# Kernel tuning notes

Measured on AMD Instinct MI355X. Metric: run time of the kernel, lower is better.

## Reference

```python
import jax, jax.numpy as jnp
import numpy as np
from functools import partial

L, B, D_IN, D_MODEL, D_OUT, D_STATE = 2048, 8, 128, 256, 32, 16
D_INNER, DT_RANK, K_CONV = 2 * D_MODEL, D_MODEL // 16, 4
LOG2PI = float(np.log(2.0 * np.pi))


def setup_inputs() -> dict:
    key = jax.random.key(0)
    ks = jax.random.split(key, 16)
    sc = 0.02
    inp = {
        "s": jax.random.normal(ks[0], (L, B, D_IN), jnp.float32),
        "a": jax.random.normal(ks[1], (L, B, D_OUT), jnp.float32),
        # embedding linear
        "W_emb": jax.random.normal(ks[2], (D_IN, D_MODEL), jnp.float32) * sc,
        "b_emb": jnp.zeros((D_MODEL,), jnp.float32),
        # mamba block params
        "norm_w": jnp.ones((D_MODEL,), jnp.float32),
        "W_in": jax.random.normal(ks[3], (D_MODEL, 2 * D_INNER), jnp.float32) * sc,
        "conv_w": jax.random.normal(ks[4], (D_INNER, 1, K_CONV), jnp.float32) * sc,
        "conv_b": jnp.zeros((D_INNER,), jnp.float32),
        "W_x": jax.random.normal(ks[5], (D_INNER, DT_RANK + 2 * D_STATE), jnp.float32) * sc,
        "W_dt": jax.random.normal(ks[6], (DT_RANK, D_INNER), jnp.float32) * sc,
        "b_dt": jnp.full((D_INNER,), -2.0, jnp.float32),  # softplus(-2) ~ small init dt
        "A_log": jnp.broadcast_to(jnp.log(jnp.arange(1, D_STATE + 1, dtype=jnp.float32)), (D_INNER, D_STATE)).copy(),
        "D": jnp.ones((D_INNER,), jnp.float32),
        "W_out": jax.random.normal(ks[7], (D_INNER, D_MODEL), jnp.float32) * sc,
        # action head + log_std
        "W_head": jax.random.normal(ks[8], (D_MODEL, D_OUT), jnp.float32) * sc,
        "b_head": jnp.zeros((D_OUT,), jnp.float32),
        "log_std": jnp.zeros((D_OUT,), jnp.float32),
    }
    return inp


def _rmsnorm(x, w, eps=1e-5):
    return x * jax.lax.rsqrt(jnp.mean(x * x, axis=-1, keepdims=True) + eps) * w


def _silu(x):
    return x * jax.nn.sigmoid(x)


def _mamba_block(x, norm_w, W_in, conv_w, conv_b, W_x, W_dt, b_dt, A_log, D, W_out):
    # x: (B, L, d_model)
    resid = x
    xn = _rmsnorm(x, norm_w)
    xz = xn @ W_in                                  # (B, L, 2*d_inner)
    xp, z = jnp.split(xz, 2, axis=-1)
    # causal depthwise conv over time
    xc = jax.lax.conv_general_dilated(
        xp.transpose(0, 2, 1), conv_w, window_strides=(1,),
        padding=[(K_CONV - 1, 0)], feature_group_count=D_INNER,
        dimension_numbers=("NCH", "OIH", "NCH"))
    xp = _silu((xc + conv_b[None, :, None]).transpose(0, 2, 1))  # (B, L, d_inner)
    # input-dependent SSM params
    x_dbl = xp @ W_x                                # (B, L, dt_rank + 2*d_state)
    dt, Bm, Cm = jnp.split(x_dbl, [DT_RANK, DT_RANK + D_STATE], axis=-1)
    dt = jax.nn.softplus(dt @ W_dt + b_dt)          # (B, L, d_inner)
    A = -jnp.exp(A_log)                             # (d_inner, d_state)

    def step(h, t):
        dt_t, B_t, C_t, x_t = t                     # (B,d_i) (B,d_s) (B,d_s) (B,d_i)
        dA = jnp.exp(dt_t[..., None] * A)           # (B, d_inner, d_state)
        dBx = (dt_t * x_t)[..., None] * B_t[:, None, :]
        h = dA * h + dBx
        y = jnp.einsum("bds,bs->bd", h, C_t)
        return h, y

    h0 = jnp.zeros((x.shape[0], D_INNER, D_STATE), x.dtype)
    tm = lambda u: jnp.moveaxis(u, 1, 0)            # time-major
    _, ys = jax.lax.scan(step, h0, (tm(dt), tm(Bm), tm(Cm), tm(xp)))
    y = jnp.moveaxis(ys, 0, 1) + xp * D             # (B, L, d_inner)
    y = y * _silu(z)
    return y @ W_out + resid


def reference(s, a, W_emb, b_emb, norm_w, W_in, conv_w, conv_b, W_x, W_dt, b_dt,
              A_log, D, W_out, W_head, b_head, log_std):
    x = s @ W_emb + b_emb                           # (L, B, d_model)
    x = x.transpose(1, 0, 2)                        # (B, L, d_model)
    x = _mamba_block(x, norm_w, W_in, conv_w, conv_b, W_x, W_dt, b_dt, A_log, D, W_out)
    x = x.transpose(1, 0, 2)                        # (L, B, d_model)
    mu = x @ W_head + b_head                        # (L, B, d_out)
    # Normal(mu, exp(log_std)).log_prob(a).sum(-1)
    z = (a - mu) * jnp.exp(-log_std)
    logp = -0.5 * z * z - log_std - 0.5 * LOG2PI
    return logp.sum(axis=-1)                        # (L, B)
```

## Files before the change

### kernel.cpp

```cpp
#include <hip/hip_runtime.h>

typedef unsigned short u16;
typedef short bf16x8 __attribute__((ext_vector_type(8)));
typedef float floatx4 __attribute__((ext_vector_type(4)));

#define LSEQ 2048
#define BB 8
#define NTOK (LSEQ*BB)
#define DMODEL 256
#define DINNER 512
#define NSEG 128
#define SEGLEN 16

__device__ __forceinline__ float siluf(float x){ return x / (1.f + __expf(-x)); }
__device__ __forceinline__ float b2f(u16 x){ return __uint_as_float(((unsigned)x) << 16); }
__device__ __forceinline__ u16 f2b(float f){
  unsigned u = __float_as_uint(f);
  unsigned r = (u + 0x7fffu + ((u >> 16) & 1u)) >> 16;
  return (u16)r;
}

__device__ __forceinline__ void compute_dA(float dt, float As0, bool uni,
    const float* __restrict__ Alog, int c, float* dA)
{
  if (uni) {
    float p = __expf(dt*As0);
    float p2 = p*p, p4 = p2*p2, p8 = p4*p4;
    dA[0]=p;      dA[1]=p2;     dA[2]=p2*p;   dA[3]=p4;
    dA[4]=p4*p;   dA[5]=p4*p2;  dA[6]=p4*p2*p;dA[7]=p8;
    dA[8]=p8*p;   dA[9]=p8*p2;  dA[10]=p8*p2*p; dA[11]=p8*p4;
    dA[12]=p8*p4*p; dA[13]=p8*p4*p2; dA[14]=p8*p4*p2*p; dA[15]=p8*p8;
  } else {
    #pragma unroll
    for (int s = 0; s < 16; ++s) dA[s] = __expf(dt * (-__expf(Alog[c*16+s])));
  }
}

__global__ __launch_bounds__(256) void prep_k(
    const float* __restrict__ Wemb, const float* __restrict__ Win,
    const float* __restrict__ Wout, const float* __restrict__ Wx,
    const float* __restrict__ Wh,
    u16* __restrict__ WTe, u16* __restrict__ WTi, u16* __restrict__ WTo,
    u16* __restrict__ WxT, u16* __restrict__ WhT)
{
  int g = blockIdx.x, tid = threadIdx.x;
  if (g < 128) {
    int idx = g*256 + tid; int n = idx >> 7, k = idx & 127;
    WTe[idx] = f2b(Wemb[(size_t)k*256 + n]);
  } else if (g < 1152) {
    int idx = (g-128)*256 + tid; int n = idx >> 8, k = idx & 255;
    WTi[idx] = f2b(Win[(size_t)k*1024 + n]);
  } else if (g < 1664) {
    int idx = (g-1152)*256 + tid; int n = idx >> 9, k = idx & 511;
    WTo[idx] = f2b(Wout[(size_t)k*256 + n]);
  } else if (g < 1760) {
    int idx = (g-1664)*256 + tid; int n = idx >> 9, k = idx & 511;
    WxT[idx] = f2b(Wx[(size_t)k*48 + n]);
  } else {
    int idx = (g-1760)*256 + tid; int j = idx >> 8, k = idx & 255;
    WhT[idx] = f2b(Wh[(size_t)k*32 + j]);
  }
}

__global__ __launch_bounds__(256) void embnorm_k(
    const float* __restrict__ s, const u16* __restrict__ WTe,
    const float* __restrict__ bemb, const float* __restrict__ nw,
    u16* __restrict__ Xb, u16* __restrict__ XNb)
{
  __shared__ u16 SH[64*264];
  __shared__ float ssq[64*4];
  __shared__ float rr[64];
  u16* As = SH;
  u16* Bs = SH + 64*40;
  const int tid = threadIdx.x;
  const int wave = tid >> 6, lane = tid & 63;
  const int quad = lane >> 4, l16 = lane & 15;
  const int m0 = blockIdx.x*64;
  const int wn = wave*64;
  const int srow = tid >> 2, sch = (tid & 3)*8;
  floatx4 acc[4][4];
  #pragma unroll
  for (int r = 0; r < 4; ++r)
    #pragma unroll
    for (int c = 0; c < 4; ++c) acc[r][c] = (floatx4){0.f,0.f,0.f,0.f};

  for (int k0 = 0; k0 < 128; k0 += 32) {
    {
      float4 v0 = *(const float4*)&s[(size_t)(m0+srow)*128 + k0 + sch];
      float4 v1 = *(const float4*)&s[(size_t)(m0+srow)*128 + k0 + sch + 4];
      __align__(16) u16 o[8];
      o[0]=f2b(v0.x); o[1]=f2b(v0.y); o[2]=f2b(v0.z); o[3]=f2b(v0.w);
      o[4]=f2b(v1.x); o[5]=f2b(v1.y); o[6]=f2b(v1.z); o[7]=f2b(v1.w);
      *(uint4*)&As[srow*40 + sch] = *(const uint4*)o;
    }
    #pragma unroll
    for (int p = 0; p < 4; ++p) {
      int row = srow + p*64;
      *(uint4*)&Bs[row*40 + sch] = *(const uint4*)&WTe[(size_t)row*128 + k0 + sch];
    }
    __syncthreads();
    bf16x8 af[4], bf[4];
    #pragma unroll
    for (int r = 0; r < 4; ++r) af[r] = *(const bf16x8*)&As[(r*16 + l16)*40 + quad*8];
    #pragma unroll
    for (int c = 0; c < 4; ++c) bf[c] = *(const bf16x8*)&Bs[(wn + c*16 + l16)*40 + quad*8];
    #pragma unroll
    for (int r = 0; r < 4; ++r)
      #pragma unroll
      for (int c = 0; c < 4; ++c)
        acc[r][c] = __builtin_amdgcn_mfma_f32_16x16x32_bf16(af[r], bf[c], acc[r][c], 0, 0, 0);
    __syncthreads();
  }
  u16* Xs = SH;
  #pragma unroll
  for (int c = 0; c < 4; ++c) {
    int n = wn + c*16 + l16;
    float bv = bemb[n];
    #pragma unroll
    for (int r = 0; r < 4; ++r)
      #pragma unroll
      for (int reg = 0; reg < 4; ++reg) {
        int ml = r*16 + quad*4 + reg;
        Xs[ml*264 + n] = f2b(acc[r][c][reg] + bv);
      }
  }
  __syncthreads();
  #pragma unroll
  for (int p = 0; p < 8; ++p) {
    int row = p*8 + (tid >> 5);
    int col = (tid & 31)*8;
    *(uint4*)&Xb[(size_t)(m0+row)*256 + col] = *(const uint4*)&Xs[row*264 + col];
  }
  const int tk = tid >> 2, q = tid & 3;
  float ss = 0.f;
  #pragma unroll
  for (int j = 0; j < 8; ++j) {
    uint4 v = *(const uint4*)&Xs[tk*264 + q*64 + j*8];
    const u16* u = (const u16*)&v;
    #pragma unroll
    for (int i = 0; i < 8; ++i) { float x = b2f(u[i]); ss += x*x; }
  }
  ssq[tk*4 + q] = ss;
  __syncthreads();
  if (q == 0)
    rr[tk] = rsqrtf((ssq[tk*4]+ssq[tk*4+1]+ssq[tk*4+2]+ssq[tk*4+3])*(1.f/DMODEL) + 1e-5f);
  __syncthreads();
  float r = rr[tk];
  #pragma unroll
  for (int j = 0; j < 8; ++j) {
    int idx = q*64 + j*8;
    uint4 v = *(const uint4*)&Xs[tk*264 + idx];
    const u16* u = (const u16*)&v;
    float4 w0 = *(const float4*)&nw[idx];
    float4 w1 = *(const float4*)&nw[idx+4];
    __align__(16) u16 o[8];
    o[0]=f2b(b2f(u[0])*r*w0.x); o[1]=f2b(b2f(u[1])*r*w0.y);
    o[2]=f2b(b2f(u[2])*r*w0.z); o[3]=f2b(b2f(u[3])*r*w0.w);
    o[4]=f2b(b2f(u[4])*r*w1.x); o[5]=f2b(b2f(u[5])*r*w1.y);
    o[6]=f2b(b2f(u[6])*r*w1.z); o[7]=f2b(b2f(u[7])*r*w1.w);
    *(uint4*)&XNb[(size_t)(m0+tk)*256 + idx] = *(const uint4*)o;
  }
}

template<int K>
__global__ __launch_bounds__(256) void gemm_mfma(
    const u16* __restrict__ Ab, const u16* __restrict__ WT,
    u16* __restrict__ Cv, int N)
{
  __shared__ u16 SH[2*128*72];
  u16* As = SH;
  u16* Bs = SH + 128*72;
  const int tid = threadIdx.x;
  const int wave = tid >> 6, lane = tid & 63;
  const int quad = lane >> 4, l16 = lane & 15;
  const int bm0 = blockIdx.x*128, bn0 = blockIdx.y*128;
  const int wm = (wave & 1)*64, wn = (wave >> 1)*64;
  const int srow = tid >> 3, sch = (tid & 7)*8;
  floatx4 acc[4][4];
  #pragma unroll
  for (int r = 0; r < 4; ++r)
    #pragma unroll
    for (int c = 0; c < 4; ++c) acc[r][c] = (floatx4){0.f,0.f,0.f,0.f};

  for (int k0 = 0; k0 < K; k0 += 64) {
    #pragma unroll
    for (int p = 0; p < 4; ++p) {
      int row = srow + p*32;
      *(uint4*)&As[row*72 + sch] = *(const uint4*)&Ab[(size_t)(bm0+row)*K + k0 + sch];
      *(uint4*)&Bs[row*72 + sch] = *(const uint4*)&WT[(size_t)(bn0+row)*K + k0 + sch];
    }
    __syncthreads();
    #pragma unroll
    for (int ks = 0; ks < 2; ++ks) {
      bf16x8 af[4], bf[4];
      #pragma unroll
      for (int r = 0; r < 4; ++r)
        af[r] = *(const bf16x8*)&As[(wm + r*16 + l16)*72 + ks*32 + quad*8];
      #pragma unroll
      for (int c = 0; c < 4; ++c)
        bf[c] = *(const bf16x8*)&Bs[(wn + c*16 + l16)*72 + ks*32 + quad*8];
      #pragma unroll
      for (int r = 0; r < 4; ++r)
        #pragma unroll
        for (int c = 0; c < 4; ++c)
          acc[r][c] = __builtin_amdgcn_mfma_f32_16x16x32_bf16(af[r], bf[c], acc[r][c], 0, 0, 0);
    }
    __syncthreads();
  }
  u16* Cs = SH;
  #pragma unroll
  for (int c = 0; c < 4; ++c) {
    int nl = wn + c*16 + l16;
    #pragma unroll
    for (int r = 0; r < 4; ++r)
      #pragma unroll
      for (int reg = 0; reg < 4; ++reg) {
        int ml = wm + r*16 + quad*4 + reg;
        Cs[ml*136 + nl] = f2b(acc[r][c][reg]);
      }
  }
  __syncthreads();
  #pragma unroll
  for (int p = 0; p < 8; ++p) {
    int row = p*16 + (tid >> 4);
    int col = (tid & 15)*8;
    uint4 v = *(const uint4*)&Cs[row*136 + col];
    *(uint4*)&Cv[(size_t)(bm0+row)*N + bn0 + col] = v;
  }
}

__global__ __launch_bounds__(256) void xdblBC_k(const u16* __restrict__ XZb,
    const float* __restrict__ cw, const float* __restrict__ cb,
    const u16* __restrict__ WxT,
    float* __restrict__ BM, float* __restrict__ CM, float* __restrict__ DTR)
{
  __shared__ u16 As[64*40];
  __shared__ u16 Ws[48*40];
  __shared__ float CWs[512*4];
  __shared__ float CBs[512];
  const int tid = threadIdx.x;
  const int wave = tid >> 6, lane = tid & 63;
  const int quad = lane >> 4, l16 = lane & 15;
  const int m0 = blockIdx.x*64;
  const int srow = tid >> 2, sch = (tid & 3)*8;
  const int n = m0 + srow;
  for (int e = tid; e < 2048; e += 256) CWs[e] = cw[e];
  for (int e = tid; e < 512;  e += 256) CBs[e] = cb[e];
  floatx4 acc[3];
  #pragma unroll
  for (int j = 0; j < 3; ++j) acc[j] = (floatx4){0.f,0.f,0.f,0.f};
  __syncthreads();
  const bf16x8 z8 = {0,0,0,0,0,0,0,0};
  for (int k0 = 0; k0 < DINNER; k0 += 32) {
    bf16x8 t3 = *(const bf16x8*)&XZb[(size_t)n*1024 + k0 + sch];
    bf16x8 t2 = z8, t1 = z8, t0v = z8;
    if (n >= 8)  t2  = *(const bf16x8*)&XZb[(size_t)(n-8)*1024  + k0 + sch];
    if (n >= 16) t1  = *(const bf16x8*)&XZb[(size_t)(n-16)*1024 + k0 + sch];
    if (n >= 24) t0v = *(const bf16x8*)&XZb[(size_t)(n-24)*1024 + k0 + sch];
    __align__(16) u16 outa[8];
    #pragma unroll
    for (int j = 0; j < 8; ++j) {
      int c = k0 + sch + j;
      float4 wv = *(const float4*)&CWs[c*4];
      float xc = CBs[c] + wv.x*b2f((u16)t0v[j]) + wv.y*b2f((u16)t1[j])
               + wv.z*b2f((u16)t2[j]) + wv.w*b2f((u16)t3[j]);
      outa[j] = f2b(siluf(xc));
    }
    *(uint4*)&As[srow*40 + sch] = *(const uint4*)outa;
    if (tid < 192) {
      int wr = tid >> 2;
      *(uint4*)&Ws[wr*40 + sch] = *(const uint4*)&WxT[(size_t)wr*512 + k0 + sch];
    }
    __syncthreads();
    bf16x8 af = *(const bf16x8*)&As[(wave*16 + l16)*40 + quad*8];
    #pragma unroll
    for (int j = 0; j < 3; ++j) {
      bf16x8 bf = *(const bf16x8*)&Ws[(j*16 + l16)*40 + quad*8];
      acc[j] = __builtin_amdgcn_mfma_f32_16x16x32_bf16(af, bf, acc[j], 0, 0, 0);
    }
    __syncthreads();
  }
  const int tok0 = m0 + wave*16;
  #pragma unroll
  for (int reg = 0; reg < 4; ++reg) {
    size_t t = (size_t)(tok0 + quad*4 + reg);
    BM[t*16 + l16]  = acc[1][reg];
    CM[t*16 + l16]  = acc[2][reg];
    DTR[t*16 + l16] = acc[0][reg];
  }
}

__global__ __launch_bounds__(256) void scanA_k(const float* __restrict__ DTR,
    const u16* __restrict__ XZb, const float* __restrict__ BM,
    const float* __restrict__ cw, const float* __restrict__ cb,
    const float* __restrict__ Wdt, const float* __restrict__ bdt,
    const float* __restrict__ Alog, u16* __restrict__ HENDb, float* __restrict__ DTS,
    unsigned* __restrict__ DXb)
{
  __shared__ float ROWa[SEGLEN*16];
  __shared__ float ROWb[SEGLEN*16];
  const int tid = threadIdx.x;
  const int seg = blockIdx.x, b = blockIdx.y, half = blockIdx.z;
  const int c = half*256 + tid;
  const int t0 = seg*SEGLEN;
  const size_t base = (size_t)t0*BB + b;
  {
    int t = tid >> 4, j = tid & 15;
    size_t off = (base + (size_t)t*BB)*16 + j;
    ROWa[tid] = BM[off];
    ROWb[tid] = DTR[off];
  }
  float As0 = -__expf(Alog[c*16]);
  bool uni = true;
  #pragma unroll
  for (int s = 1; s < 16; ++s) {
    float Av = -__expf(Alog[c*16+s]);
    uni = uni && (fabsf(Av - As0*(float)(s+1)) <= 1e-4f*(float)(s+1));
  }
  float wdt[16];
  #pragma unroll
  for (int r = 0; r < 16; ++r) wdt[r] = Wdt[r*DINNER + c];
  const float bd = bdt[c];
  const float4 cwv = *(const float4*)&cw[c*4];
  const float cbv = cb[c];
  float h[16];
  #pragma unroll
  for (int s = 0; s < 16; ++s) h[s] = 0.f;
  float dts = 0.f;
  const u16* xzp = XZb + base*1024 + c;
  float w0 = (t0 >= 3) ? b2f(xzp[-(size_t)3*BB*1024]) : 0.f;
  float w1 = (t0 >= 2) ? b2f(xzp[-(size_t)2*BB*1024]) : 0.f;
  float w2 = (t0 >= 1) ? b2f(xzp[-(size_t)1*BB*1024]) : 0.f;
  float xz = b2f(xzp[0]);
  __syncthreads();
  for (int t = 0; t < SEGLEN; ++t) {
    float xzn = (t+1 < SEGLEN) ? b2f(xzp[(size_t)(t+1)*BB*1024]) : 0.f;
    float dsum = bd;
    #pragma unroll
    for (int r = 0; r < 16; ++r) dsum = fmaf(ROWb[t*16+r], wdt[r], dsum);
    float dt = (dsum > 20.f) ? dsum : __logf(1.f + __expf(dsum));
    float xp = siluf(cbv + cwv.x*w0 + cwv.y*w1 + cwv.z*w2 + cwv.w*xz);
    w0 = w1; w1 = w2; w2 = xz; xz = xzn;
    dts += dt;
    DXb[(((size_t)(t0+t)*BB + b)*DINNER + c)] = ((unsigned)f2b(xp) << 16) | f2b(dt);
    float dtx = dt * xp;
    float dA[16];
    compute_dA(dt, As0, uni, Alog, c, dA);
    #pragma unroll
    for (int s = 0; s < 16; ++s)
      h[s] = fmaf(dA[s], h[s], dtx * ROWa[t*16+s]);
  }
  u16* hp = &HENDb[(((size_t)seg*BB + b)*DINNER + c)*16];
  #pragma unroll
  for (int q = 0; q < 2; ++q) {
    ushort4 v0, v1;
    v0.x = f2b(h[q*8+0]); v0.y = f2b(h[q*8+1]); v0.z = f2b(h[q*8+2]); v0.w = f2b(h[q*8+3]);
    v1.x = f2b(h[q*8+4]); v1.y = f2b(h[q*8+5]); v1.z = f2b(h[q*8+6]); v1.w = f2b(h[q*8+7]);
    *(ushort4*)&hp[q*8]     = v0;
    *(ushort4*)&hp[q*8 + 4] = v1;
  }
  DTS[((size_t)seg*BB + b)*DINNER + c] = dts;
}

__global__ __launch_bounds__(256) void stitch_k(u16* __restrict__ HENDb,
    const float* __restrict__ DTS, const float* __restrict__ Alog)
{
  int g = blockIdx.x*256 + threadIdx.x;
  int b = g >> 13;
  int rem = g & 8191;
  int cidx = rem >> 4;
  float A = -__expf(Alog[rem]);
  float h0 = 0.f;
  for (int k = 0; k < NSEG; ++k) {
    size_t idx = (((size_t)k*BB + b) << 13) + rem;
    float hend = b2f(HENDb[idx]);
    HENDb[idx] = f2b(h0);
    float dts = DTS[((size_t)k*BB + b)*DINNER + cidx];
    h0 = fmaf(__expf(dts*A), h0, hend);
  }
}

__global__ __launch_bounds__(256) void scanC_k(const unsigned* __restrict__ DXb,
    const u16* __restrict__ XZb, const float* __restrict__ BM, const float* __restrict__ CM,
    const float* __restrict__ Alog, const float* __restrict__ Dp,
    const u16* __restrict__ H0b, u16* __restrict__ YGb)
{
  __shared__ float ROWa[SEGLEN*16];
  __shared__ float ROWc[SEGLEN*16];
  const int tid = threadIdx.x;
  const int seg = blockIdx.x, b = blockIdx.y, half = blockIdx.z;
  const int c = half*256 + tid;
  const int t0 = seg*SEGLEN;
  const size_t base = (size_t)t0*BB + b;
  {
    int t = tid >> 4, j = tid & 15;
    size_t off = (base + (size_t)t*BB)*16 + j;
    ROWa[tid] = BM[off];
    ROWc[tid] = CM[off];
  }
  float As0 = -__expf(Alog[c*16]);
  bool uni = true;
  #pragma unroll
  for (int s = 1; s < 16; ++s) {
    float Av = -__expf(Alog[c*16+s]);
    uni = uni && (fabsf(Av - As0*(float)(s+1)) <= 1e-4f*(float)(s+1));
  }
  float h[16];
  const u16* hp = &H0b[(((size_t)seg*BB + b)*DINNER + c)*16];
  #pragma unroll
  for (int q = 0; q < 4; ++q) {
    ushort4 hv = *(const ushort4*)&hp[q*4];
    h[q*4+0]=b2f(hv.x); h[q*4+1]=b2f(hv.y); h[q*4+2]=b2f(hv.z); h[q*4+3]=b2f(hv.w);
  }
  const float Dv = Dp[c];
  const unsigned* dxp = DXb + base*DINNER + c;
  const u16* zp  = XZb + base*1024 + DINNER + c;
  u16*       ygp = YGb + base*DINNER + c;
  unsigned dx = dxp[0];
  float zg = b2f(zp[0]);
  __syncthreads();
  for (int t = 0; t < SEGLEN; ++t) {
    unsigned dxn = 0; float zgn = 0.f;
    if (t+1 < SEGLEN) {
      dxn = dxp[(size_t)(t+1)*BB*DINNER];
      zgn = b2f(zp[(size_t)(t+1)*BB*1024]);
    }
    float dt = __uint_as_float(dx << 16);
    float xp = __uint_as_float(dx & 0xffff0000u);
    float dtx = dt * xp;
    float dA[16];
    compute_dA(dt, As0, uni, Alog, c, dA);
    float y0 = 0.f, y1 = 0.f, y2 = 0.f, y3 = 0.f;
    #pragma unroll
    for (int q = 0; q < 4; ++q) {
      h[q*4+0] = fmaf(dA[q*4+0], h[q*4+0], dtx*ROWa[t*16+q*4+0]);
      h[q*4+1] = fmaf(dA[q*4+1], h[q*4+1], dtx*ROWa[t*16+q*4+1]);
      h[q*4+2] = fmaf(dA[q*4+2], h[q*4+2], dtx*ROWa[t*16+q*4+2]);
      h[q*4+3] = fmaf(dA[q*4+3], h[q*4+3], dtx*ROWa[t*16+q*4+3]);
      y0 = fmaf(h[q*4+0], ROWc[t*16+q*4+0], y0);
      y1 = fmaf(h[q*4+1], ROWc[t*16+q*4+1], y1);
      y2 = fmaf(h[q*4+2], ROWc[t*16+q*4+2], y2);
      y3 = fmaf(h[q*4+3], ROWc[t*16+q*4+3], y3);
    }
    float y = (y0+y1) + (y2+y3);
    ygp[(size_t)t*BB*DINNER] = f2b((y + xp*Dv) * siluf(zg));
    dx = dxn; zg = zgn;
  }
}

__global__ __launch_bounds__(256) void outhead_k(const u16* __restrict__ YGb,
    const u16* __restrict__ WTo, const u16* __restrict__ Xb,
    const u16* __restrict__ WhT, const float* __restrict__ bh,
    const float* __restrict__ lstd, const float* __restrict__ a,
    float* __restrict__ out)
{
  __shared__ u16 SH[(64+256)*72];
  u16* As = SH;
  u16* Bs = SH + 64*72;
  const int tid = threadIdx.x;
  const int wave = tid >> 6, lane = tid & 63;
  const int quad = lane >> 4, l16 = lane & 15;
  const int m0 = blockIdx.x*64;
  const int n0 = wave*64;
  const int srow = tid >> 3, sch = (tid & 7)*8;
  floatx4 acc[4][4];
  #pragma unroll
  for (int r = 0; r < 4; ++r)
    #pragma unroll
    for (int c = 0; c < 4; ++c) acc[r][c] = (floatx4){0.f,0.f,0.f,0.f};

  for (int k0 = 0; k0 < DINNER; k0 += 64) {
    #pragma unroll
    for (int p = 0; p < 2; ++p) {
      int row = srow + p*32;
      *(uint4*)&As[row*72 + sch] = *(const uint4*)&YGb[(size_t)(m0+row)*DINNER + k0 + sch];
    }
    #pragma unroll
    for (int p = 0; p < 8; ++p) {
      int row = srow + p*32;
      *(uint4*)&Bs[row*72 + sch] = *(const uint4*)&WTo[(size_t)row*DINNER + k0 + sch];
    }
    __syncthreads();
    #pragma unroll
    for (int ks = 0; ks < 2; ++ks) {
      bf16x8 af[4], bf[4];
      #pragma unroll
      for (int r = 0; r < 4; ++r)
        af[r] = *(const bf16x8*)&As[(r*16 + l16)*72 + ks*32 + quad*8];
      #pragma unroll
      for (int c = 0; c < 4; ++c)
        bf[c] = *(const bf16x8*)&Bs[(n0 + c*16 + l16)*72 + ks*32 + quad*8];
      #pragma unroll
      for (int r = 0; r < 4; ++r)
        #pragma unroll
        for (int c = 0; c < 4; ++c)
          acc[r][c] = __builtin_amdgcn_mfma_f32_16x16x32_bf16(af[r], bf[c], acc[r][c], 0, 0, 0);
    }
    __syncthreads();
  }
  u16* Xs = SH;
  #pragma unroll
  for (int p = 0; p < 8; ++p) {
    int row = p*8 + (tid >> 5);
    int col = (tid & 31)*8;
    *(uint4*)&Xs[row*264 + col] = *(const uint4*)&Xb[(size_t)(m0+row)*256 + col];
  }
  __syncthreads();
  #pragma unroll
  for (int c = 0; c < 4; ++c) {
    int n = n0 + c*16 + l16;
    #pragma unroll
    for (int r = 0; r < 4; ++r) {
      #pragma unroll
      for (int reg = 0; reg < 4; ++reg) {
        int ml = r*16 + quad*4 + reg;
        Xs[ml*264 + n] = f2b(acc[r][c][reg] + b2f(Xs[ml*264 + n]));
      }
    }
  }
  __syncthreads();
  floatx4 mu[2];
  mu[0] = (floatx4){0.f,0.f,0.f,0.f};
  mu[1] = (floatx4){0.f,0.f,0.f,0.f};
  #pragma unroll
  for (int k0 = 0; k0 < DMODEL; k0 += 32) {
    bf16x8 axf = *(const bf16x8*)&Xs[(wave*16 + l16)*264 + k0 + quad*8];
    #pragma unroll
    for (int nt = 0; nt < 2; ++nt) {
      bf16x8 bwf = *(const bf16x8*)(WhT + (size_t)(nt*16 + l16)*DMODEL + k0 + quad*8);
      mu[nt] = __builtin_amdgcn_mfma_f32_16x16x32_bf16(axf, bwf, mu[nt], 0, 0, 0);
    }
  }
  float ls0 = lstd[l16],      els0 = __expf(-ls0), bh0 = bh[l16];
  float ls1 = lstd[16 + l16], els1 = __expf(-ls1), bh1 = bh[16 + l16];
  #pragma unroll
  for (int reg = 0; reg < 4; ++reg) {
    int tok = m0 + wave*16 + quad*4 + reg;
    float m0v = mu[0][reg] + bh0;
    float m1v = mu[1][reg] + bh1;
    float z0 = (a[(size_t)tok*32 + l16]      - m0v) * els0;
    float z1 = (a[(size_t)tok*32 + 16 + l16] - m1v) * els1;
    float t = (-0.5f*z0*z0 - ls0) + (-0.5f*z1*z1 - ls1) - 2.f*0.91893853320467274f;
    t += __shfl_xor(t, 1);
    t += __shfl_xor(t, 2);
    t += __shfl_xor(t, 4);
    t += __shfl_xor(t, 8);
    if (l16 == 0) out[tok] = t;
  }
}

extern "C" void kernel_launch(void* const* d_in, const int* in_sizes, int n_in,
                              void* d_out, int out_size, void* d_ws, size_t ws_size,
                              hipStream_t stream)
{
  const float* s    = (const float*)d_in[0];
  const float* a    = (const float*)d_in[1];
  const float* Wemb = (const float*)d_in[2];
  const float* bemb = (const float*)d_in[3];
  const float* nw   = (const float*)d_in[4];
  const float* Win  = (const float*)d_in[5];
  const float* cw   = (const float*)d_in[6];
  const float* cb   = (const float*)d_in[7];
  const float* Wx   = (const float*)d_in[8];
  const float* Wdt  = (const float*)d_in[9];
  const float* bdt  = (const float*)d_in[10];
  const float* Alog = (const float*)d_in[11];
  const float* Dp   = (const float*)d_in[12];
  const float* Wout = (const float*)d_in[13];
  const float* Wh   = (const float*)d_in[14];
  const float* bh   = (const float*)d_in[15];
  const float* lstd = (const float*)d_in[16];

  u16*   Xb   = (u16*)d_ws;
  u16*   XZb  = Xb  + (size_t)NTOK*DMODEL;
  u16*   XNb  = XZb + (size_t)NTOK*1024;
  u16*   YGb  = XNb + (size_t)NTOK*DMODEL;
  u16*   WTe  = YGb + (size_t)NTOK*DINNER;
  u16*   WTi  = WTe + 256*128;
  u16*   WTo  = WTi + 1024*256;
  u16*   WxT  = WTo + 256*512;
  u16*   WhT  = WxT + 48*512;
  u16*   HENDb= WhT + 32*256;
  unsigned* DXb = (unsigned*)(HENDb + (size_t)NSEG*BB*DINNER*16);
  float* BM   = (float*)(DXb + (size_t)NTOK*DINNER);
  float* CM   = BM + (size_t)NTOK*16;
  float* DTR  = CM + (size_t)NTOK*16;
  float* DTS  = DTR + (size_t)NTOK*16;
  float* out  = (float*)d_out;

  prep_k        <<<1792,        256, 0, stream>>>(Wemb, Win, Wout, Wx, Wh,
                                                  WTe, WTi, WTo, WxT, WhT);
  embnorm_k     <<<256,         256, 0, stream>>>(s, WTe, bemb, nw, Xb, XNb);
  gemm_mfma<256><<<dim3(128,8), 256, 0, stream>>>(XNb, WTi, XZb, 1024);
  xdblBC_k      <<<256,         256, 0, stream>>>(XZb, cw, cb, WxT, BM, CM, DTR);
  scanA_k       <<<dim3(NSEG,BB,2), 256, 0, stream>>>(DTR, XZb, BM, cw, cb, Wdt, bdt,
                                                      Alog, HENDb, DTS, DXb);
  stitch_k      <<<256,         256, 0, stream>>>(HENDb, DTS, Alog);
  scanC_k       <<<dim3(NSEG,BB,2), 256, 0, stream>>>(DXb, XZb, BM, CM,
                                                      Alog, Dp, HENDb, YGb);
  outhead_k     <<<256,         256, 0, stream>>>(YGb, WTo, Xb, WhT, bh, lstd, a, out);
}
```

Measured before the change: 243.5 us.

## Lengthen scan segments, batch stitch loads, tile weight transposes via LDS

```diff
diff --git a/kernel.cpp b/kernel.cpp
--- a/kernel.cpp
+++ b/kernel.cpp
@@ -10,7 +10,8 @@
 #define DMODEL 256
 #define DINNER 512
 #define NSEG 128
-#define SEGLEN 16
+#define SEG_N 64
+#define SEG_L 32
 
 __device__ __forceinline__ float siluf(float x){ return x / (1.f + __expf(-x)); }
 __device__ __forceinline__ float b2f(u16 x){ return __uint_as_float(((unsigned)x) << 16); }
@@ -43,21 +44,38 @@
     u16* __restrict__ WTe, u16* __restrict__ WTi, u16* __restrict__ WTo,
     u16* __restrict__ WxT, u16* __restrict__ WhT)
 {
+  __shared__ u16 T[64*66];
   int g = blockIdx.x, tid = threadIdx.x;
-  if (g < 128) {
-    int idx = g*256 + tid; int n = idx >> 7, k = idx & 127;
+  if (g < 96) {
+    const float* src; u16* dst; int n0, k0, srcld, dstld;
+    if (g < 64) {
+      int tn = g & 15, tk = g >> 4;
+      n0 = tn*64; k0 = tk*64; src = Win; dst = WTi; srcld = 1024; dstld = 256;
+    } else {
+      int g2 = g - 64;
+      int tn = g2 & 3, tk = g2 >> 2;
+      n0 = tn*64; k0 = tk*64; src = Wout; dst = WTo; srcld = 256; dstld = 512;
+    }
+    int rr = tid >> 6, cc = tid & 63;
+    #pragma unroll
+    for (int p = 0; p < 16; ++p) {
+      int kr = p*4 + rr;
+      T[kr*66 + cc] = f2b(src[(size_t)(k0+kr)*srcld + n0 + cc]);
+    }
+    __syncthreads();
+    #pragma unroll
+    for (int p = 0; p < 16; ++p) {
+      int nr = p*4 + rr;
+      dst[(size_t)(n0+nr)*dstld + k0 + cc] = T[cc*66 + nr];
+    }
+  } else if (g < 224) {
+    int idx = (g-96)*256 + tid; int n = idx >> 7, k = idx & 127;
     WTe[idx] = f2b(Wemb[(size_t)k*256 + n]);
-  } else if (g < 1152) {
-    int idx = (g-128)*256 + tid; int n = idx >> 8, k = idx & 255;
-    WTi[idx] = f2b(Win[(size_t)k*1024 + n]);
-  } else if (g < 1664) {
-    int idx = (g-1152)*256 + tid; int n = idx >> 9, k = idx & 511;
-    WTo[idx] = f2b(Wout[(size_t)k*256 + n]);
-  } else if (g < 1760) {
-    int idx = (g-1664)*256 + tid; int n = idx >> 9, k = idx & 511;
+  } else if (g < 320) {
+    int idx = (g-224)*256 + tid; int n = idx >> 9, k = idx & 511;
     WxT[idx] = f2b(Wx[(size_t)k*48 + n]);
   } else {
-    int idx = (g-1760)*256 + tid; int j = idx >> 8, k = idx & 255;
+    int idx = (g-320)*256 + tid; int j = idx >> 8, k = idx & 255;
     WhT[idx] = f2b(Wh[(size_t)k*32 + j]);
   }
 }
@@ -297,18 +315,18 @@
     const float* __restrict__ Alog, u16* __restrict__ HENDb, float* __restrict__ DTS,
     unsigned* __restrict__ DXb)
 {
-  __shared__ float ROWa[SEGLEN*16];
-  __shared__ float ROWb[SEGLEN*16];
+  __shared__ float ROWa[SEG_L*16];
+  __shared__ float ROWb[SEG_L*16];
   const int tid = threadIdx.x;
   const int seg = blockIdx.x, b = blockIdx.y, half = blockIdx.z;
   const int c = half*256 + tid;
-  const int t0 = seg*SEGLEN;
+  const int t0 = seg*SEG_L;
   const size_t base = (size_t)t0*BB + b;
-  {
-    int t = tid >> 4, j = tid & 15;
+  for (int idx = tid; idx < SEG_L*16; idx += 256) {
+    int t = idx >> 4, j = idx & 15;
     size_t off = (base + (size_t)t*BB)*16 + j;
-    ROWa[tid] = BM[off];
-    ROWb[tid] = DTR[off];
+    ROWa[idx] = BM[off];
+    ROWb[idx] = DTR[off];
   }
   float As0 = -__expf(Alog[c*16]);
   bool uni = true;
@@ -333,8 +351,8 @@
   float w2 = (t0 >= 1) ? b2f(xzp[-(size_t)1*BB*1024]) : 0.f;
   float xz = b2f(xzp[0]);
   __syncthreads();
-  for (int t = 0; t < SEGLEN; ++t) {
-    float xzn = (t+1 < SEGLEN) ? b2f(xzp[(size_t)(t+1)*BB*1024]) : 0.f;
+  for (int t = 0; t < SEG_L; ++t) {
+    float xzn = (t+1 < SEG_L) ? b2f(xzp[(size_t)(t+1)*BB*1024]) : 0.f;
     float dsum = bd;
     #pragma unroll
     for (int r = 0; r < 16; ++r) dsum = fmaf(ROWb[t*16+r], wdt[r], dsum);
@@ -371,12 +389,20 @@
   int cidx = rem >> 4;
   float A = -__expf(Alog[rem]);
   float h0 = 0.f;
-  for (int k = 0; k < NSEG; ++k) {
-    size_t idx = (((size_t)k*BB + b) << 13) + rem;
-    float hend = b2f(HENDb[idx]);
-    HENDb[idx] = f2b(h0);
-    float dts = DTS[((size_t)k*BB + b)*DINNER + cidx];
-    h0 = fmaf(__expf(dts*A), h0, hend);
+  for (int k = 0; k < SEG_N; k += 4) {
+    float he[4], ds[4];
+    #pragma unroll
+    for (int u = 0; u < 4; ++u) {
+      size_t idx = (((size_t)(k+u)*BB + b) << 13) + rem;
+      he[u] = b2f(HENDb[idx]);
+      ds[u] = DTS[((size_t)(k+u)*BB + b)*DINNER + cidx];
+    }
+    #pragma unroll
+    for (int u = 0; u < 4; ++u) {
+      size_t idx = (((size_t)(k+u)*BB + b) << 13) + rem;
+      HENDb[idx] = f2b(h0);
+      h0 = fmaf(__expf(ds[u]*A), h0, he[u]);
+    }
   }
 }
 
@@ -385,18 +411,18 @@
     const float* __restrict__ Alog, const float* __restrict__ Dp,
     const u16* __restrict__ H0b, u16* __restrict__ YGb)
 {
-  __shared__ float ROWa[SEGLEN*16];
-  __shared__ float ROWc[SEGLEN*16];
+  __shared__ float ROWa[SEG_L*16];
+  __shared__ float ROWc[SEG_L*16];
   const int tid = threadIdx.x;
   const int seg = blockIdx.x, b = blockIdx.y, half = blockIdx.z;
   const int c = half*256 + tid;
-  const int t0 = seg*SEGLEN;
+  const int t0 = seg*SEG_L;
   const size_t base = (size_t)t0*BB + b;
-  {
-    int t = tid >> 4, j = tid & 15;
+  for (int idx = tid; idx < SEG_L*16; idx += 256) {
+    int t = idx >> 4, j = idx & 15;
     size_t off = (base + (size_t)t*BB)*16 + j;
-    ROWa[tid] = BM[off];
-    ROWc[tid] = CM[off];
+    ROWa[idx] = BM[off];
+    ROWc[idx] = CM[off];
   }
   float As0 = -__expf(Alog[c*16]);
   bool uni = true;
@@ -419,9 +445,9 @@
   unsigned dx = dxp[0];
   float zg = b2f(zp[0]);
   __syncthreads();
-  for (int t = 0; t < SEGLEN; ++t) {
+  for (int t = 0; t < SEG_L; ++t) {
     unsigned dxn = 0; float zgn = 0.f;
-    if (t+1 < SEGLEN) {
+    if (t+1 < SEG_L) {
       dxn = dxp[(size_t)(t+1)*BB*DINNER];
       zgn = b2f(zp[(size_t)(t+1)*BB*1024]);
     }
@@ -588,15 +614,15 @@
   float* DTS  = DTR + (size_t)NTOK*16;
   float* out  = (float*)d_out;
 
-  prep_k        <<<1792,        256, 0, stream>>>(Wemb, Win, Wout, Wx, Wh,
+  prep_k        <<<352,         256, 0, stream>>>(Wemb, Win, Wout, Wx, Wh,
                                                   WTe, WTi, WTo, WxT, WhT);
   embnorm_k     <<<256,         256, 0, stream>>>(s, WTe, bemb, nw, Xb, XNb);
   gemm_mfma<256><<<dim3(128,8), 256, 0, stream>>>(XNb, WTi, XZb, 1024);
   xdblBC_k      <<<256,         256, 0, stream>>>(XZb, cw, cb, WxT, BM, CM, DTR);
-  scanA_k       <<<dim3(NSEG,BB,2), 256, 0, stream>>>(DTR, XZb, BM, cw, cb, Wdt, bdt,
-                                                      Alog, HENDb, DTS, DXb);
+  scanA_k       <<<dim3(SEG_N,BB,2), 256, 0, stream>>>(DTR, XZb, BM, cw, cb, Wdt, bdt,
+                                                       Alog, HENDb, DTS, DXb);
   stitch_k      <<<256,         256, 0, stream>>>(HENDb, DTS, Alog);
-  scanC_k       <<<dim3(NSEG,BB,2), 256, 0, stream>>>(DXb, XZb, BM, CM,
-                                                      Alog, Dp, HENDb, YGb);
+  scanC_k       <<<dim3(SEG_N,BB,2), 256, 0, stream>>>(DXb, XZb, BM, CM,
+                                                       Alog, Dp, HENDb, YGb);
   outhead_k     <<<256,         256, 0, stream>>>(YGb, WTo, Xb, WhT, bh, lstd, a, out);
 }
```

Result: no change. 239.5 us (-1.7%).
